# Optimization experiments

Hardware: AMD Instinct MI355X
Metric: run time of the kernel (lower is better)

## Reference

```python
import jax, jax.numpy as jnp
import numpy as np

D = 1024

def setup_inputs() -> dict:
    key = jax.random.key(0)
    k1, k2, k3, k4 = jax.random.split(key, 4)
    context = jax.random.normal(k1, (32, 2048, D), dtype=jnp.float32)
    # nn.Linear(dim, dim, bias=False): weight [D, D], applied as x @ W.T
    W = jax.random.normal(k2, (D, D), dtype=jnp.float32) / np.sqrt(D)
    # nn.Linear(dim, 1): weight [1, D], bias [1]
    v = jax.random.normal(k3, (D,), dtype=jnp.float32) / np.sqrt(D)
    b = jax.random.normal(k4, (), dtype=jnp.float32) * 0.01
    return {"context": context, "W": W, "v": v, "b": b}

def reference(context, W, v, b):
    # context: [B, S, D]
    h = jnp.tanh(jnp.einsum('bsd,ed->bse', context, W))      # [B, S, D]
    attn_logits = jnp.einsum('bsd,d->bs', h, v) + b          # [B, S]
    attn = jax.nn.softmax(attn_logits, axis=-1)              # softmax over sourceL
    weighted_context = jnp.einsum('bs,bsd->bd', attn, context)
    return weighted_context, attn
```

## Files before the change

kernel.cpp:

```cpp
#include <hip/hip_runtime.h>
#include <stdint.h>

#define BDIM 32
#define SDIM 2048
#define DDIM 1024
#define MDIM (BDIM * SDIM)

typedef __bf16 bf16x8 __attribute__((ext_vector_type(8)));
typedef float  f32x4  __attribute__((ext_vector_type(4)));


__device__ inline unsigned short f2bf(float f) {
  union { float f; unsigned u; } un; un.f = f;
  unsigned r = un.u + 0x7fffu + ((un.u >> 16) & 1u);
  return (unsigned short)(r >> 16);
}

__device__ inline float fast_tanh(float x) {
  float e = __expf(2.0f * x);
  return 1.0f - 2.0f / (e + 1.0f);
}

__device__ inline void gl_lds16(const unsigned short* g, unsigned short* l) {
  __builtin_amdgcn_global_load_lds(
      (__attribute__((address_space(1))) unsigned int*)(void*)(uintptr_t)g,
      (__attribute__((address_space(3))) unsigned int*)l,
      16, 0, 0);
}


__global__ __launch_bounds__(256) void cvt_kernel(const float* __restrict__ src,
                                                  unsigned short* __restrict__ dst) {
  size_t i = (size_t)blockIdx.x * 256 + threadIdx.x;
  const float4* s4 = (const float4*)src;
  float4 a = s4[2 * i];
  float4 b = s4[2 * i + 1];
  uint4 o;
  o.x = (unsigned)f2bf(a.x) | ((unsigned)f2bf(a.y) << 16);
  o.y = (unsigned)f2bf(a.z) | ((unsigned)f2bf(a.w) << 16);
  o.z = (unsigned)f2bf(b.x) | ((unsigned)f2bf(b.y) << 16);
  o.w = (unsigned)f2bf(b.z) | ((unsigned)f2bf(b.w) << 16);
  ((uint4*)dst)[i] = o;
}


__global__ __launch_bounds__(256) void gemm_logits(
    const unsigned short* __restrict__ A,
    const unsigned short* __restrict__ Bw,
    const float* __restrict__ v,
    float* __restrict__ logits)
{
  __shared__ __align__(16) unsigned short Al[128 * 32];
  __shared__ __align__(16) unsigned short Bl[128 * 32];

  const int t  = threadIdx.x;
  const int mt = blockIdx.x >> 3;
  const int nt = blockIdx.x & 7;
  const int m0 = mt * 128;
  const int n0 = nt * 128;
  const int w    = t >> 6;
  const int lane = t & 63;
  const int wm = (w >> 1) * 64;
  const int wn = (w & 1) * 64;
  const int c = lane & 15;
  const int q = lane >> 4;

  float vv[4];
#pragma unroll
  for (int ni = 0; ni < 4; ++ni) vv[ni] = v[n0 + wn + ni * 16 + c];

  f32x4 acc[4][4] = {};

  const int srow = t >> 2;
  const int skel = (t & 3) * 8;
  const unsigned short* ga0 = A  + (size_t)(m0 + srow) * DDIM + skel;
  const unsigned short* ga1 = A  + (size_t)(m0 + 64 + srow) * DDIM + skel;
  const unsigned short* gb0 = Bw + (size_t)(n0 + srow) * DDIM + skel;
  const unsigned short* gb1 = Bw + (size_t)(n0 + 64 + srow) * DDIM + skel;
  unsigned short* la0 = Al + w * 512;
  unsigned short* la1 = Al + 2048 + w * 512;
  unsigned short* lb0 = Bl + w * 512;
  unsigned short* lb1 = Bl + 2048 + w * 512;

  for (int kt = 0; kt < 32; ++kt) {
    const int k0 = kt * 32;
    gl_lds16(ga0 + k0, la0);
    gl_lds16(ga1 + k0, la1);
    gl_lds16(gb0 + k0, lb0);
    gl_lds16(gb1 + k0, lb1);
    __syncthreads();

    bf16x8 af[4], bfr[4];
#pragma unroll
    for (int mi = 0; mi < 4; ++mi)
      af[mi] = *(const bf16x8*)&Al[(wm + mi * 16 + c) * 32 + q * 8];
#pragma unroll
    for (int ni = 0; ni < 4; ++ni)
      bfr[ni] = *(const bf16x8*)&Bl[(wn + ni * 16 + c) * 32 + q * 8];

#pragma unroll
    for (int mi = 0; mi < 4; ++mi)
#pragma unroll
      for (int ni = 0; ni < 4; ++ni)
        acc[mi][ni] = __builtin_amdgcn_mfma_f32_16x16x32_bf16(
            af[mi], bfr[ni], acc[mi][ni], 0, 0, 0);

    __syncthreads();
  }

#pragma unroll
  for (int mi = 0; mi < 4; ++mi) {
    float p0 = 0.f, p1 = 0.f, p2 = 0.f, p3 = 0.f;
#pragma unroll
    for (int ni = 0; ni < 4; ++ni) {
      const float vvn = vv[ni];
      p0 += fast_tanh(acc[mi][ni][0]) * vvn;
      p1 += fast_tanh(acc[mi][ni][1]) * vvn;
      p2 += fast_tanh(acc[mi][ni][2]) * vvn;
      p3 += fast_tanh(acc[mi][ni][3]) * vvn;
    }
#pragma unroll
    for (int mask = 1; mask <= 8; mask <<= 1) {
      p0 += __shfl_xor(p0, mask);
      p1 += __shfl_xor(p1, mask);
      p2 += __shfl_xor(p2, mask);
      p3 += __shfl_xor(p3, mask);
    }
    if (c == 0) {
      float* lp = logits + (m0 + wm + mi * 16 + q * 4);
      atomicAdd(lp + 0, p0);
      atomicAdd(lp + 1, p1);
      atomicAdd(lp + 2, p2);
      atomicAdd(lp + 3, p3);
    }
  }
}


__global__ __launch_bounds__(256) void softmax_kernel(float* __restrict__ la) {
  const int b = blockIdx.x;
  const int t = threadIdx.x;
  float* p = la + (size_t)b * SDIM;
  float x[8];
#pragma unroll
  for (int i = 0; i < 8; ++i) x[i] = p[i * 256 + t];
  float m = x[0];
#pragma unroll
  for (int i = 1; i < 8; ++i) m = fmaxf(m, x[i]);
#pragma unroll
  for (int mask = 1; mask < 64; mask <<= 1) m = fmaxf(m, __shfl_xor(m, mask));
  __shared__ float redm[4], reds[4];
  const int w = t >> 6, lane = t & 63;
  if (lane == 0) redm[w] = m;
  __syncthreads();
  m = fmaxf(fmaxf(redm[0], redm[1]), fmaxf(redm[2], redm[3]));
  float e[8];
  float s = 0.f;
#pragma unroll
  for (int i = 0; i < 8; ++i) { e[i] = __expf(x[i] - m); s += e[i]; }
#pragma unroll
  for (int mask = 1; mask < 64; mask <<= 1) s += __shfl_xor(s, mask);
  if (lane == 0) reds[w] = s;
  __syncthreads();
  s = reds[0] + reds[1] + reds[2] + reds[3];
  const float inv = 1.0f / s;
#pragma unroll
  for (int i = 0; i < 8; ++i) p[i * 256 + t] = e[i] * inv;
}


__global__ __launch_bounds__(256) void wsum_kernel(const float* __restrict__ ctx,
                                                   const float* __restrict__ attn,
                                                   float* __restrict__ wc) {
  const int b  = blockIdx.x >> 4;
  const int sc = blockIdx.x & 15;
  const int t  = threadIdx.x;
  const float* cp = ctx + ((size_t)b * SDIM + sc * 128) * DDIM + t * 4;
  const float* ap = attn + (size_t)b * SDIM + sc * 128;
  float4 acc = {0.f, 0.f, 0.f, 0.f};
  for (int s = 0; s < 128; ++s) {
    const float a = ap[s];
    const float4 cv = *(const float4*)(cp + (size_t)s * DDIM);
    acc.x += a * cv.x; acc.y += a * cv.y; acc.z += a * cv.z; acc.w += a * cv.w;
  }
  float* o = wc + (size_t)b * DDIM + t * 4;
  atomicAdd(o + 0, acc.x);
  atomicAdd(o + 1, acc.y);
  atomicAdd(o + 2, acc.z);
  atomicAdd(o + 3, acc.w);
}


extern "C" void kernel_launch(void* const* d_in, const int* in_sizes, int n_in,
                              void* d_out, int out_size, void* d_ws, size_t ws_size,
                              hipStream_t stream) {
  const float* ctx = (const float*)d_in[0];
  const float* W   = (const float*)d_in[1];
  const float* v   = (const float*)d_in[2];

  float* out_wc   = (float*)d_out;
  float* out_attn = out_wc + BDIM * DDIM;

  unsigned short* ctx_bf = (unsigned short*)d_ws;
  unsigned short* W_bf   = ctx_bf + (size_t)MDIM * DDIM;

  hipMemsetAsync(d_out, 0, (size_t)out_size * sizeof(float), stream);

  cvt_kernel<<<(MDIM * DDIM) / (256 * 8), 256, 0, stream>>>(ctx, ctx_bf);
  cvt_kernel<<<(DDIM * DDIM) / (256 * 8), 256, 0, stream>>>(W, W_bf);
  gemm_logits<<<(MDIM / 128) * (DDIM / 128), 256, 0, stream>>>(ctx_bf, W_bf, v, out_attn);
  softmax_kernel<<<BDIM, 256, 0, stream>>>(out_attn);
  wsum_kernel<<<BDIM * 16, 256, 0, stream>>>(ctx, out_attn, out_wc);
}
```

Baseline: 619.4 us.

## Fuse context bf16 conversion into GEMM and loop over N tiles per block

The GEMM kernel now handles a full 128-row strip across all eight N tiles. On the first N tile it converts the fp32 context to bf16 itself, writing the result both to LDS and to a workspace copy that later N tiles reload. This removes the separate conversion pass, the memset and the logit atomics, and the LDS uses a 64-wide K tile with an XOR swizzle. The weighted-sum atomics are replaced by per-chunk partial sums plus a reduction kernel. The cost is fewer blocks (512), each doing more serial work, so parallelism is lower.

Result: slower. 634.1 us (+2.4%).

```diff
diff --git a/kernel.cpp b/kernel.cpp
--- a/kernel.cpp
+++ b/kernel.cpp
@@ -44,94 +44,121 @@
 }
 
 
-__global__ __launch_bounds__(256) void gemm_logits(
-    const unsigned short* __restrict__ A,
-    const unsigned short* __restrict__ Bw,
+__global__ __launch_bounds__(256, 2) void gemm_logits(
+    const float* __restrict__ ctx,
+    const unsigned short* __restrict__ Wb,
+    unsigned short* __restrict__ Abf,
     const float* __restrict__ v,
     float* __restrict__ logits)
 {
-  __shared__ __align__(16) unsigned short Al[128 * 32];
-  __shared__ __align__(16) unsigned short Bl[128 * 32];
-
-  const int t  = threadIdx.x;
-  const int mt = blockIdx.x >> 3;
-  const int nt = blockIdx.x & 7;
-  const int m0 = mt * 128;
-  const int n0 = nt * 128;
+  __shared__ __align__(16) unsigned short Al[128 * 64];
+  __shared__ __align__(16) unsigned short Wl[128 * 64];
+
+  const int t    = threadIdx.x;
+  const int m0   = blockIdx.x * 128;
   const int w    = t >> 6;
   const int lane = t & 63;
-  const int wm = (w >> 1) * 64;
-  const int wn = (w & 1) * 64;
-  const int c = lane & 15;
-  const int q = lane >> 4;
-
-  float vv[4];
-#pragma unroll
-  for (int ni = 0; ni < 4; ++ni) vv[ni] = v[n0 + wn + ni * 16 + c];
-
-  f32x4 acc[4][4] = {};
-
-  const int srow = t >> 2;
-  const int skel = (t & 3) * 8;
-  const unsigned short* ga0 = A  + (size_t)(m0 + srow) * DDIM + skel;
-  const unsigned short* ga1 = A  + (size_t)(m0 + 64 + srow) * DDIM + skel;
-  const unsigned short* gb0 = Bw + (size_t)(n0 + srow) * DDIM + skel;
-  const unsigned short* gb1 = Bw + (size_t)(n0 + 64 + srow) * DDIM + skel;
-  unsigned short* la0 = Al + w * 512;
-  unsigned short* la1 = Al + 2048 + w * 512;
-  unsigned short* lb0 = Bl + w * 512;
-  unsigned short* lb1 = Bl + 2048 + w * 512;
-
-  for (int kt = 0; kt < 32; ++kt) {
-    const int k0 = kt * 32;
-    gl_lds16(ga0 + k0, la0);
-    gl_lds16(ga1 + k0, la1);
-    gl_lds16(gb0 + k0, lb0);
-    gl_lds16(gb1 + k0, lb1);
-    __syncthreads();
-
-    bf16x8 af[4], bfr[4];
-#pragma unroll
-    for (int mi = 0; mi < 4; ++mi)
-      af[mi] = *(const bf16x8*)&Al[(wm + mi * 16 + c) * 32 + q * 8];
-#pragma unroll
-    for (int ni = 0; ni < 4; ++ni)
-      bfr[ni] = *(const bf16x8*)&Bl[(wn + ni * 16 + c) * 32 + q * 8];
-
-#pragma unroll
-    for (int mi = 0; mi < 4; ++mi)
-#pragma unroll
-      for (int ni = 0; ni < 4; ++ni)
-        acc[mi][ni] = __builtin_amdgcn_mfma_f32_16x16x32_bf16(
-            af[mi], bfr[ni], acc[mi][ni], 0, 0, 0);
-
-    __syncthreads();
+  const int c    = lane & 15;
+  const int q    = lane >> 4;
+  const int wm   = w * 32;
+
+  const int rt   = t >> 3;
+  const int sA   = t & 7;
+  const int sx   = rt & 7;
+  const int psl  = sA ^ sx;
+
+  float p[2][4] = {};
+
+  for (int nt = 0; nt < 8; ++nt) {
+    const int n0 = nt * 128;
+    f32x4 acc[2][8] = {};
+
+    for (int kt = 0; kt < 16; ++kt) {
+      const int k0 = kt * 64;
+
+      if (nt == 0) {
+#pragma unroll
+        for (int j = 0; j < 4; ++j) {
+          const int row = j * 32 + rt;
+          const float* g = ctx + (size_t)(m0 + row) * DDIM + k0 + sA * 8;
+          float4 a = *(const float4*)g;
+          float4 b = *(const float4*)(g + 4);
+          bf16x8 cv;
+          cv[0] = (__bf16)a.x; cv[1] = (__bf16)a.y;
+          cv[2] = (__bf16)a.z; cv[3] = (__bf16)a.w;
+          cv[4] = (__bf16)b.x; cv[5] = (__bf16)b.y;
+          cv[6] = (__bf16)b.z; cv[7] = (__bf16)b.w;
+          *(bf16x8*)&Al[row * 64 + psl * 8] = cv;
+          *(bf16x8*)&Abf[(size_t)(m0 + row) * DDIM + k0 + sA * 8] = cv;
+        }
+      } else {
+#pragma unroll
+        for (int r = 0; r < 4; ++r) {
+          const int row = r * 32 + rt;
+          gl_lds16(Abf + (size_t)(m0 + row) * DDIM + k0 + psl * 8,
+                   Al + (r * 256 + (t & 192)) * 8);
+        }
+      }
+#pragma unroll
+      for (int r = 0; r < 4; ++r) {
+        const int row = r * 32 + rt;
+        gl_lds16(Wb + (size_t)(n0 + row) * DDIM + k0 + psl * 8,
+                 Wl + (r * 256 + (t & 192)) * 8);
+      }
+      __syncthreads();
+
+#pragma unroll
+      for (int kk = 0; kk < 2; ++kk) {
+        bf16x8 af[2], bw[8];
+#pragma unroll
+        for (int mi = 0; mi < 2; ++mi) {
+          const int row = wm + mi * 16 + c;
+          af[mi] = *(const bf16x8*)&Al[row * 64 + (((kk * 4 + q) ^ (c & 7)) * 8)];
+        }
+#pragma unroll
+        for (int ni = 0; ni < 8; ++ni) {
+          const int row = ni * 16 + c;
+          bw[ni] = *(const bf16x8*)&Wl[row * 64 + (((kk * 4 + q) ^ (c & 7)) * 8)];
+        }
+#pragma unroll
+        for (int mi = 0; mi < 2; ++mi)
+#pragma unroll
+          for (int ni = 0; ni < 8; ++ni)
+            acc[mi][ni] = __builtin_amdgcn_mfma_f32_16x16x32_bf16(
+                af[mi], bw[ni], acc[mi][ni], 0, 0, 0);
+      }
+      __syncthreads();
+    }
+
+#pragma unroll
+    for (int ni = 0; ni < 8; ++ni) {
+      const float vvn = v[n0 + ni * 16 + c];
+#pragma unroll
+      for (int mi = 0; mi < 2; ++mi) {
+        p[mi][0] += fast_tanh(acc[mi][ni][0]) * vvn;
+        p[mi][1] += fast_tanh(acc[mi][ni][1]) * vvn;
+        p[mi][2] += fast_tanh(acc[mi][ni][2]) * vvn;
+        p[mi][3] += fast_tanh(acc[mi][ni][3]) * vvn;
+      }
+    }
   }
 
 #pragma unroll
-  for (int mi = 0; mi < 4; ++mi) {
-    float p0 = 0.f, p1 = 0.f, p2 = 0.f, p3 = 0.f;
-#pragma unroll
-    for (int ni = 0; ni < 4; ++ni) {
-      const float vvn = vv[ni];
-      p0 += fast_tanh(acc[mi][ni][0]) * vvn;
-      p1 += fast_tanh(acc[mi][ni][1]) * vvn;
-      p2 += fast_tanh(acc[mi][ni][2]) * vvn;
-      p3 += fast_tanh(acc[mi][ni][3]) * vvn;
-    }
-#pragma unroll
-    for (int mask = 1; mask <= 8; mask <<= 1) {
-      p0 += __shfl_xor(p0, mask);
-      p1 += __shfl_xor(p1, mask);
-      p2 += __shfl_xor(p2, mask);
-      p3 += __shfl_xor(p3, mask);
-    }
-    if (c == 0) {
-      float* lp = logits + (m0 + wm + mi * 16 + q * 4);
-      atomicAdd(lp + 0, p0);
-      atomicAdd(lp + 1, p1);
-      atomicAdd(lp + 2, p2);
-      atomicAdd(lp + 3, p3);
+  for (int mi = 0; mi < 2; ++mi)
+#pragma unroll
+    for (int r = 0; r < 4; ++r) {
+      float x = p[mi][r];
+      x += __shfl_xor(x, 1);
+      x += __shfl_xor(x, 2);
+      x += __shfl_xor(x, 4);
+      x += __shfl_xor(x, 8);
+      p[mi][r] = x;
+    }
+  if (c == 0) {
+#pragma unroll
+    for (int mi = 0; mi < 2; ++mi) {
+      float4 o = {p[mi][0], p[mi][1], p[mi][2], p[mi][3]};
+      *(float4*)(logits + m0 + wm + mi * 16 + q * 4) = o;
     }
   }
 }
@@ -169,9 +196,9 @@
 }
 
 
-__global__ __launch_bounds__(256) void wsum_kernel(const float* __restrict__ ctx,
-                                                   const float* __restrict__ attn,
-                                                   float* __restrict__ wc) {
+__global__ __launch_bounds__(256) void wsum_part(const float* __restrict__ ctx,
+                                                 const float* __restrict__ attn,
+                                                 float* __restrict__ part) {
   const int b  = blockIdx.x >> 4;
   const int sc = blockIdx.x & 15;
   const int t  = threadIdx.x;
@@ -183,11 +210,18 @@
     const float4 cv = *(const float4*)(cp + (size_t)s * DDIM);
     acc.x += a * cv.x; acc.y += a * cv.y; acc.z += a * cv.z; acc.w += a * cv.w;
   }
-  float* o = wc + (size_t)b * DDIM + t * 4;
-  atomicAdd(o + 0, acc.x);
-  atomicAdd(o + 1, acc.y);
-  atomicAdd(o + 2, acc.z);
-  atomicAdd(o + 3, acc.w);
+  *(float4*)(part + (size_t)blockIdx.x * DDIM + t * 4) = acc;
+}
+
+
+__global__ __launch_bounds__(256) void wsum_reduce(const float* __restrict__ part,
+                                                   float* __restrict__ wc) {
+  const int b = blockIdx.x >> 2;
+  const int d = (blockIdx.x & 3) * 256 + threadIdx.x;
+  float s = 0.f;
+#pragma unroll
+  for (int sc = 0; sc < 16; ++sc) s += part[(size_t)(b * 16 + sc) * DDIM + d];
+  wc[(size_t)b * DDIM + d] = s;
 }
 
 
@@ -201,14 +235,13 @@
   float* out_wc   = (float*)d_out;
   float* out_attn = out_wc + BDIM * DDIM;
 
-  unsigned short* ctx_bf = (unsigned short*)d_ws;
-  unsigned short* W_bf   = ctx_bf + (size_t)MDIM * DDIM;
-
-  hipMemsetAsync(d_out, 0, (size_t)out_size * sizeof(float), stream);
-
-  cvt_kernel<<<(MDIM * DDIM) / (256 * 8), 256, 0, stream>>>(ctx, ctx_bf);
+  unsigned short* W_bf   = (unsigned short*)d_ws;
+  unsigned short* ctx_bf = W_bf + (size_t)DDIM * DDIM;
+  float* part = (float*)(void*)ctx_bf;
+
   cvt_kernel<<<(DDIM * DDIM) / (256 * 8), 256, 0, stream>>>(W, W_bf);
-  gemm_logits<<<(MDIM / 128) * (DDIM / 128), 256, 0, stream>>>(ctx_bf, W_bf, v, out_attn);
+  gemm_logits<<<MDIM / 128, 256, 0, stream>>>(ctx, W_bf, ctx_bf, v, out_attn);
   softmax_kernel<<<BDIM, 256, 0, stream>>>(out_attn);
-  wsum_kernel<<<BDIM * 16, 256, 0, stream>>>(ctx, out_attn, out_wc);
-}
+  wsum_part<<<BDIM * 16, 256, 0, stream>>>(ctx, out_attn, part);
+  wsum_reduce<<<(BDIM * DDIM) / 256, 256, 0, stream>>>(part, out_wc);
+}
```

## Deepen GEMM K-tile with XOR-swizzled LDS, remap blocks, split weighted-sum reduction

Applied to the files above, without the earlier changes.

The GEMM now loads a 64-wide K tile per iteration, half as many barrier rounds, and stores it in LDS with an XOR swizzle to avoid bank conflicts on fragment reads. Block indices are remapped so consecutive blocks share the same N tile across different M tiles. The weighted sum is split into a partial kernel with more blocks and a deterministic reduce kernel, replacing float atomics. The partials reuse the bf16 context workspace, and the memset now covers only the attention region. This doubles LDS per block, which may lower occupancy.

New measurement: 626.9 us. About the same (+1.2%).

```diff
diff --git a/kernel.cpp b/kernel.cpp
--- a/kernel.cpp
+++ b/kernel.cpp
@@ -50,20 +50,21 @@
     const float* __restrict__ v,
     float* __restrict__ logits)
 {
-  __shared__ __align__(16) unsigned short Al[128 * 32];
-  __shared__ __align__(16) unsigned short Bl[128 * 32];
+  __shared__ __align__(16) unsigned short Al[128 * 64];
+  __shared__ __align__(16) unsigned short Wl[128 * 64];
 
   const int t  = threadIdx.x;
-  const int mt = blockIdx.x >> 3;
-  const int nt = blockIdx.x & 7;
+  const int l  = (blockIdx.x & 7) * 512 + (blockIdx.x >> 3);
+  const int mt = l >> 3;
+  const int nt = l & 7;
   const int m0 = mt * 128;
   const int n0 = nt * 128;
   const int w    = t >> 6;
   const int lane = t & 63;
+  const int c = lane & 15;
+  const int q = lane >> 4;
   const int wm = (w >> 1) * 64;
   const int wn = (w & 1) * 64;
-  const int c = lane & 15;
-  const int q = lane >> 4;
 
   float vv[4];
 #pragma unroll
@@ -71,40 +72,41 @@
 
   f32x4 acc[4][4] = {};
 
-  const int srow = t >> 2;
-  const int skel = (t & 3) * 8;
-  const unsigned short* ga0 = A  + (size_t)(m0 + srow) * DDIM + skel;
-  const unsigned short* ga1 = A  + (size_t)(m0 + 64 + srow) * DDIM + skel;
-  const unsigned short* gb0 = Bw + (size_t)(n0 + srow) * DDIM + skel;
-  const unsigned short* gb1 = Bw + (size_t)(n0 + 64 + srow) * DDIM + skel;
-  unsigned short* la0 = Al + w * 512;
-  unsigned short* la1 = Al + 2048 + w * 512;
-  unsigned short* lb0 = Bl + w * 512;
-  unsigned short* lb1 = Bl + 2048 + w * 512;
-
-  for (int kt = 0; kt < 32; ++kt) {
-    const int k0 = kt * 32;
-    gl_lds16(ga0 + k0, la0);
-    gl_lds16(ga1 + k0, la1);
-    gl_lds16(gb0 + k0, lb0);
-    gl_lds16(gb1 + k0, lb1);
+  const int rt  = t >> 3;
+  const int sA  = t & 7;
+  const int psl = sA ^ (rt & 7);
+  const unsigned short* ga = A  + (size_t)(m0 + rt) * DDIM + psl * 8;
+  const unsigned short* gb = Bw + (size_t)(n0 + rt) * DDIM + psl * 8;
+  unsigned short* lab = Al + (size_t)(t & 192) * 8;
+  unsigned short* lwb = Wl + (size_t)(t & 192) * 8;
+
+  for (int kt = 0; kt < 16; ++kt) {
+    const int k0 = kt * 64;
+#pragma unroll
+    for (int r = 0; r < 4; ++r)
+      gl_lds16(ga + (size_t)(r * 32) * DDIM + k0, lab + r * 2048);
+#pragma unroll
+    for (int r = 0; r < 4; ++r)
+      gl_lds16(gb + (size_t)(r * 32) * DDIM + k0, lwb + r * 2048);
     __syncthreads();
 
-    bf16x8 af[4], bfr[4];
-#pragma unroll
-    for (int mi = 0; mi < 4; ++mi)
-      af[mi] = *(const bf16x8*)&Al[(wm + mi * 16 + c) * 32 + q * 8];
-#pragma unroll
-    for (int ni = 0; ni < 4; ++ni)
-      bfr[ni] = *(const bf16x8*)&Bl[(wn + ni * 16 + c) * 32 + q * 8];
-
-#pragma unroll
-    for (int mi = 0; mi < 4; ++mi)
+#pragma unroll
+    for (int kk = 0; kk < 2; ++kk) {
+      bf16x8 af[4], bfr[4];
+      const int slot = ((kk * 4 + q) ^ (c & 7)) * 8;
+#pragma unroll
+      for (int mi = 0; mi < 4; ++mi)
+        af[mi] = *(const bf16x8*)&Al[(wm + mi * 16 + c) * 64 + slot];
 #pragma unroll
       for (int ni = 0; ni < 4; ++ni)
-        acc[mi][ni] = __builtin_amdgcn_mfma_f32_16x16x32_bf16(
-            af[mi], bfr[ni], acc[mi][ni], 0, 0, 0);
-
+        bfr[ni] = *(const bf16x8*)&Wl[(wn + ni * 16 + c) * 64 + slot];
+#pragma unroll
+      for (int mi = 0; mi < 4; ++mi)
+#pragma unroll
+        for (int ni = 0; ni < 4; ++ni)
+          acc[mi][ni] = __builtin_amdgcn_mfma_f32_16x16x32_bf16(
+              af[mi], bfr[ni], acc[mi][ni], 0, 0, 0);
+    }
     __syncthreads();
   }
 
@@ -169,25 +171,34 @@
 }
 
 
-__global__ __launch_bounds__(256) void wsum_kernel(const float* __restrict__ ctx,
-                                                   const float* __restrict__ attn,
-                                                   float* __restrict__ wc) {
-  const int b  = blockIdx.x >> 4;
-  const int sc = blockIdx.x & 15;
+__global__ __launch_bounds__(256) void wsum_part(const float* __restrict__ ctx,
+                                                 const float* __restrict__ attn,
+                                                 float* __restrict__ part) {
+  const int b  = blockIdx.x >> 6;
+  const int sc = blockIdx.x & 63;
   const int t  = threadIdx.x;
-  const float* cp = ctx + ((size_t)b * SDIM + sc * 128) * DDIM + t * 4;
-  const float* ap = attn + (size_t)b * SDIM + sc * 128;
+  const float* cp = ctx + ((size_t)b * SDIM + sc * 32) * DDIM + t * 4;
+  const float* ap = attn + (size_t)b * SDIM + sc * 32;
   float4 acc = {0.f, 0.f, 0.f, 0.f};
-  for (int s = 0; s < 128; ++s) {
+#pragma unroll 4
+  for (int s = 0; s < 32; ++s) {
     const float a = ap[s];
     const float4 cv = *(const float4*)(cp + (size_t)s * DDIM);
     acc.x += a * cv.x; acc.y += a * cv.y; acc.z += a * cv.z; acc.w += a * cv.w;
   }
-  float* o = wc + (size_t)b * DDIM + t * 4;
-  atomicAdd(o + 0, acc.x);
-  atomicAdd(o + 1, acc.y);
-  atomicAdd(o + 2, acc.z);
-  atomicAdd(o + 3, acc.w);
+  *(float4*)(part + (size_t)blockIdx.x * DDIM + t * 4) = acc;
+}
+
+
+__global__ __launch_bounds__(256) void wsum_reduce(const float* __restrict__ part,
+                                                   float* __restrict__ wc) {
+  const int b = blockIdx.x >> 2;
+  const int d = (blockIdx.x & 3) * 256 + threadIdx.x;
+  float s = 0.f;
+#pragma unroll
+  for (int sc = 0; sc < 64; ++sc)
+    s += part[((size_t)b * 64 + sc) * DDIM + d];
+  wc[(size_t)b * DDIM + d] = s;
 }
 
 
@@ -201,14 +212,16 @@
   float* out_wc   = (float*)d_out;
   float* out_attn = out_wc + BDIM * DDIM;
 
-  unsigned short* ctx_bf = (unsigned short*)d_ws;
-  unsigned short* W_bf   = ctx_bf + (size_t)MDIM * DDIM;
-
-  hipMemsetAsync(d_out, 0, (size_t)out_size * sizeof(float), stream);
-
+  unsigned short* W_bf   = (unsigned short*)d_ws;
+  unsigned short* ctx_bf = W_bf + (size_t)DDIM * DDIM;
+  float* part = (float*)(void*)ctx_bf;
+
+  hipMemsetAsync(out_attn, 0, (size_t)BDIM * SDIM * sizeof(float), stream);
+
+  cvt_kernel<<<(DDIM * DDIM) / (256 * 8), 256, 0, stream>>>(W, W_bf);
   cvt_kernel<<<(MDIM * DDIM) / (256 * 8), 256, 0, stream>>>(ctx, ctx_bf);
-  cvt_kernel<<<(DDIM * DDIM) / (256 * 8), 256, 0, stream>>>(W, W_bf);
   gemm_logits<<<(MDIM / 128) * (DDIM / 128), 256, 0, stream>>>(ctx_bf, W_bf, v, out_attn);
   softmax_kernel<<<BDIM, 256, 0, stream>>>(out_attn);
-  wsum_kernel<<<BDIM * 16, 256, 0, stream>>>(ctx, out_attn, out_wc);
-}
+  wsum_part<<<BDIM * 64, 256, 0, stream>>>(ctx, out_attn, part);
+  wsum_reduce<<<(BDIM * DDIM) / 256, 256, 0, stream>>>(part, out_wc);
+}
```
